# Kernel optimization log

Measured on AMD Instinct MI355X. Metric: run time of the kernel, lower is better.

Reference implementation:

```python
import jax, jax.numpy as jnp
import numpy as np
import math

B, S, D = 1, 1024, 4096
H, HD, KVH = 32, 128, 8
R, FF = 16, 14336
EPS = 1e-5


def setup_inputs() -> dict:
    key = jax.random.key(0)
    ks = jax.random.split(key, 32)
    def nrm(i, shape, scale):
        return jax.random.normal(ks[i], shape, dtype=jnp.float32) * scale
    inp = {}
    inp["x"] = nrm(0, (B, S, D), 0.5)
    inp["norm_w1"] = jnp.ones((D,), jnp.float32)
    inp["norm_w2"] = jnp.ones((D,), jnp.float32)
    # rotary embedding tables (Mistral theta=10000)
    inv_freq = 1.0 / (10000.0 ** (jnp.arange(0, HD, 2, dtype=jnp.float32) / HD))
    freqs = jnp.outer(jnp.arange(S, dtype=jnp.float32), inv_freq)
    emb = jnp.concatenate([freqs, freqs], axis=-1)  # [S, HD]
    inp["cos"] = jnp.cos(emb)
    inp["sin"] = jnp.sin(emb)
    causal = jnp.tril(jnp.ones((S, S), dtype=bool))
    inp["mask"] = jnp.where(causal, 0.0, -1e9).astype(jnp.float32)[None, None]  # [1,1,S,S]
    w_shapes = {"wq": (D, D), "wk": (KVH * HD, D), "wv": (KVH * HD, D),
                "wo": (D, D), "wg": (FF, D), "wu": (FF, D), "wd": (D, FF)}
    i = 1
    for name, shp in w_shapes.items():
        inp[name] = nrm(i, shp, 0.02); i += 1
        dout, din = shp
        inp["la_" + name[1]] = nrm(i, (din, R), 0.02); i += 1
        inp["lb_" + name[1]] = nrm(i, (R, dout), 0.02); i += 1
    inp["num_heads"] = H
    inp["head_dim"] = HD
    inp["num_kv_heads"] = KVH
    return inp


def _rms(x, w):
    # rmsnorm_forward with eps=1e-5, weight only
    return x * jax.lax.rsqrt(jnp.mean(x * x, axis=-1, keepdims=True) + EPS) * w


def _lora(x, W, la, lb):
    # dequantized base weight [out,in] applied as x @ W.T, plus low-rank delta
    return x @ W.T + (x @ la) @ lb


def _rope(x, cos, sin):
    # x: [B, h, S, HD]; rotate_half convention
    x1, x2 = jnp.split(x, 2, axis=-1)
    rot = jnp.concatenate([-x2, x1], axis=-1)
    return x * cos[None, None] + rot * sin[None, None]


def _layer(x, norm_w1, norm_w2, cos, sin, mask,
           wq, la_q, lb_q, wk, la_k, lb_k, wv, la_v, lb_v, wo, la_o, lb_o,
           wg, la_g, lb_g, wu, la_u, lb_u, wd, la_d, lb_d,
           num_heads, head_dim, num_kv_heads):
    b, s, d = x.shape
    n_rep = num_heads // num_kv_heads
    xn1 = _rms(x, norm_w1)
    q = _lora(xn1, wq, la_q, lb_q).reshape(b, s, num_heads, head_dim).transpose(0, 2, 1, 3)
    k = _lora(xn1, wk, la_k, lb_k).reshape(b, s, num_kv_heads, head_dim).transpose(0, 2, 1, 3)
    v = _lora(xn1, wv, la_v, lb_v).reshape(b, s, num_kv_heads, head_dim).transpose(0, 2, 1, 3)
    q = _rope(q, cos, sin)
    k = _rope(k, cos, sin)
    k = jnp.repeat(k, n_rep, axis=1)
    v = jnp.repeat(v, n_rep, axis=1)
    scores = jnp.einsum("bhqd,bhkd->bhqk", q, k) / math.sqrt(head_dim) + mask
    a = jax.nn.softmax(scores, axis=-1)
    o = jnp.einsum("bhqk,bhkd->bhqd", a, v).transpose(0, 2, 1, 3).reshape(b, s, d)
    o = _lora(o, wo, la_o, lb_o)
    x_med = x + o
    xn2 = _rms(x_med, norm_w2)
    gate = _lora(xn2, wg, la_g, lb_g)
    up = _lora(xn2, wu, la_u, lb_u)
    h = jax.nn.silu(gate) * up
    down = _lora(h, wd, la_d, lb_d)
    return x_med + down


def reference(x, norm_w1, norm_w2, cos, sin, mask,
              wq, la_q, lb_q, wk, la_k, lb_k, wv, la_v, lb_v, wo, la_o, lb_o,
              wg, la_g, lb_g, wu, la_u, lb_u, wd, la_d, lb_d,
              num_heads, head_dim, num_kv_heads):
    return _layer(x, norm_w1, norm_w2, cos, sin, mask,
                  wq, la_q, lb_q, wk, la_k, lb_k, wv, la_v, lb_v, wo, la_o, lb_o,
                  wg, la_g, lb_g, wu, la_u, lb_u, wd, la_d, lb_d,
                  num_heads, head_dim, num_kv_heads)
```

## Files before the change

kernel.cpp:

```cpp
#include <hip/hip_runtime.h>
#include <hip/hip_bf16.h>
#include <math.h>

#define SEQ 1024
#define DIM 4096
#define NH 32
#define HD 128
#define NKVH 8
#define FF 14336
#define LR 16

typedef __attribute__((ext_vector_type(8))) short bf16x8;
typedef __attribute__((ext_vector_type(4))) float f32x4;
typedef __attribute__((ext_vector_type(4))) ushort ushort4v;

__device__ __forceinline__ ushort f2bf(float f) {
  union { float f; unsigned u; } v; v.f = f;
  unsigned r = (v.u + 0x7FFFu + ((v.u >> 16) & 1u)) >> 16;
  return (ushort)r;
}
__device__ __forceinline__ float bf2f(ushort h) {
  union { unsigned u; float f; } v; v.u = ((unsigned)h) << 16;
  return v.f;
}

__device__ __forceinline__ void gload_lds16(const void* g, void* l) {
  __builtin_amdgcn_global_load_lds(
      (const __attribute__((address_space(1))) void*)g,
      (__attribute__((address_space(3))) void*)l, 16, 0, 0);
}

__global__ __launch_bounds__(256) void rmsnorm_kernel(const float* __restrict__ x,
                                                      const float* __restrict__ w,
                                                      ushort* __restrict__ out) {
  int row = blockIdx.x;
  int tid = threadIdx.x;
  const float* xr = x + (size_t)row * DIM;
  float vals[16];
  float s = 0.f;
#pragma unroll
  for (int c = 0; c < 4; c++) {
    float4 v = *(const float4*)&xr[(tid + c * 256) * 4];
    vals[c * 4 + 0] = v.x; vals[c * 4 + 1] = v.y;
    vals[c * 4 + 2] = v.z; vals[c * 4 + 3] = v.w;
    s += v.x * v.x + v.y * v.y + v.z * v.z + v.w * v.w;
  }
#pragma unroll
  for (int off = 32; off >= 1; off >>= 1) s += __shfl_down(s, off);
  __shared__ float wsum[4];
  __shared__ float scale_s;
  int lane = tid & 63, wv = tid >> 6;
  if (lane == 0) wsum[wv] = s;
  __syncthreads();
  if (tid == 0) {
    float t = wsum[0] + wsum[1] + wsum[2] + wsum[3];
    scale_s = rsqrtf(t / (float)DIM + 1e-5f);
  }
  __syncthreads();
  float scale = scale_s;
  ushort* orow = out + (size_t)row * DIM;
#pragma unroll
  for (int c = 0; c < 4; c++) {
    int base = (tid + c * 256) * 4;
    float4 wv4 = *(const float4*)&w[base];
    ushort4v ov;
    ov.x = f2bf(vals[c * 4 + 0] * scale * wv4.x);
    ov.y = f2bf(vals[c * 4 + 1] * scale * wv4.y);
    ov.z = f2bf(vals[c * 4 + 2] * scale * wv4.z);
    ov.w = f2bf(vals[c * 4 + 3] * scale * wv4.w);
    *(ushort4v*)&orow[base] = ov;
  }
}

template <int NL>
__global__ __launch_bounds__(256) void lora_a_kernel(
    const ushort* __restrict__ A,
    const float* __restrict__ la0, const float* __restrict__ la1,
    const float* __restrict__ la2,
    ushort* __restrict__ t0, ushort* __restrict__ t1, ushort* __restrict__ t2,
    int K) {
  int m = blockIdx.x, i = threadIdx.x;
  float acc[NL][16];
#pragma unroll
  for (int l = 0; l < NL; l++)
#pragma unroll
    for (int n = 0; n < 16; n++) acc[l][n] = 0.f;

  const ushort* Arow = A + (size_t)m * K;
  int nc = K >> 8;
  for (int c = 0; c < nc; c++) {
    int k = c * 256 + i;
    float a = bf2f(Arow[k]);
#pragma unroll
    for (int l = 0; l < NL; l++) {
      const float* lap = (l == 0 ? la0 : (l == 1 ? la1 : la2)) + (size_t)k * 16;
#pragma unroll
      for (int q = 0; q < 4; q++) {
        float4 lv = *(const float4*)&lap[q * 4];
        acc[l][q * 4 + 0] += a * lv.x;
        acc[l][q * 4 + 1] += a * lv.y;
        acc[l][q * 4 + 2] += a * lv.z;
        acc[l][q * 4 + 3] += a * lv.w;
      }
    }
  }

  __shared__ float red[256][17];
  __shared__ float red2[16][17];
#pragma unroll
  for (int l = 0; l < NL; l++) {
    __syncthreads();
#pragma unroll
    for (int n = 0; n < 16; n++) red[i][n] = acc[l][n];
    __syncthreads();
    {
      int g = i >> 4, n = i & 15;
      float s = 0.f;
#pragma unroll
      for (int j = 0; j < 16; j++) s += red[g * 16 + j][n];
      red2[g][n] = s;
    }
    __syncthreads();
    if (i < 16) {
      float s2 = 0.f;
#pragma unroll
      for (int g2 = 0; g2 < 16; g2++) s2 += red2[g2][i];
      ushort* tp = (l == 0 ? t0 : (l == 1 ? t1 : t2));
      tp[(size_t)m * LR + i] = f2bf(s2);
    }
  }
}

template <int WM>
__global__ __launch_bounds__(512) void gemm256_kernel(
    const ushort* __restrict__ A,
    const float* __restrict__ W0, const float* __restrict__ W1, const float* __restrict__ W2,
    const float* __restrict__ lb0, const float* __restrict__ lb1, const float* __restrict__ lb2,
    const ushort* __restrict__ t0, const ushort* __restrict__ t1, const ushort* __restrict__ t2,
    int c1, int c2, void* __restrict__ outp, int M, int N, int K, int nkp) {
  __shared__ __align__(16) ushort As[2][256 * 64];
  __shared__ __align__(16) ushort Bs[2][256 * 64];
  int tid = threadIdx.x;
  int lane = tid & 63, wave = tid >> 6;
  int wm = wave >> 2, wn = wave & 3;

  int gx = gridDim.x, gy = gridDim.y;
  int flat = blockIdx.x + gx * (blockIdx.y + gy * blockIdx.z);
  int nwg = gx * gy * gridDim.z;
  int q = nwg >> 3, r = nwg & 7;
  int xcd = flat & 7;
  int wgid = (xcd < r ? xcd * (q + 1) : r * (q + 1) + (xcd - r) * q) + (flat >> 3);
  int bx = wgid % gx;
  int tmp = wgid / gx;
  int by = tmp % gy;
  int z = tmp / gy;

  int n0 = bx * 256, m0 = by * 256;
  int k0 = z * nkp;

  const float* Wp; const float* lbp; const ushort* tp; int nseg, wseg;
  if (n0 < c1)      { Wp = W0; lbp = lb0; tp = t0; nseg = n0;      wseg = c1; }
  else if (n0 < c2) { Wp = W1; lbp = lb1; tp = t1; nseg = n0 - c1; wseg = c2 - c1; }
  else              { Wp = W2; lbp = lb2; tp = t2; nseg = n0 - c2; wseg = N - c2; }

  int srow = tid >> 3;
  int sswz = ((tid & 7) ^ (srow & 7)) * 8;
  const ushort* Ab = A + (size_t)(m0 + srow) * K + sswz;
  const float* Wbase = Wp + (size_t)(nseg + srow) * K + (tid & 7) * 8;
  int bphys = ((tid & 7) ^ (srow & 7)) * 8;

  f32x4 acc[8][4] = {};
  float4 breg[8];

#define SHALF(kt, b, h)                                                       \
  _Pragma("unroll") for (int i = 2 * (h); i < 2 * (h) + 2; i++) {             \
    gload_lds16(Ab + (size_t)(i * 64) * K + (size_t)(kt) * 64,                \
                &As[b][wave * 512 + i * 4096]);                               \
  }
#define BLOAD(kt, h)                                                          \
  {                                                                           \
    const float* gp = Wbase + (size_t)((h) * 128) * K + (size_t)(kt) * 64;    \
    breg[(h) * 4 + 0] = *(const float4*)gp;                                   \
    breg[(h) * 4 + 1] = *(const float4*)(gp + 4);                             \
    breg[(h) * 4 + 2] = *(const float4*)(gp + (size_t)64 * K);                \
    breg[(h) * 4 + 3] = *(const float4*)(gp + (size_t)64 * K + 4);            \
  }
#define WRITE_B(b)                                                            \
  _Pragma("unroll") for (int h = 0; h < 2; h++)                               \
  _Pragma("unroll") for (int j = 0; j < 2; j++) {                             \
    int rr = h * 128 + j * 64 + srow;                                         \
    float4 lo = breg[h * 4 + j * 2 + 0];                                      \
    float4 hi = breg[h * 4 + j * 2 + 1];                                      \
    bf16x8 v;                                                                 \
    v[0] = (short)f2bf(lo.x); v[1] = (short)f2bf(lo.y);                       \
    v[2] = (short)f2bf(lo.z); v[3] = (short)f2bf(lo.w);                       \
    v[4] = (short)f2bf(hi.x); v[5] = (short)f2bf(hi.y);                       \
    v[6] = (short)f2bf(hi.z); v[7] = (short)f2bf(hi.w);                       \
    *(bf16x8*)&Bs[b][rr * 64 + (((tid & 7) ^ (rr & 7))) * 8] = v;             \
  }
#define LDFRAG(buf, rr, ks) \
  (*(const bf16x8*)&(buf)[(rr) * 64 + (((ks) * 4 + (lane >> 4)) ^ ((rr) & 7)) * 8])

  BLOAD(k0, 0); BLOAD(k0, 1);
  SHALF(k0, 0, 0); SHALF(k0, 0, 1);
  asm volatile("s_waitcnt vmcnt(4)" ::: "memory");
  WRITE_B(0);
  if (nkp > 1) { BLOAD(k0 + 1, 0); BLOAD(k0 + 1, 1); }
  if (nkp > 1) asm volatile("s_waitcnt vmcnt(8)" ::: "memory");
  else         asm volatile("s_waitcnt vmcnt(0)" ::: "memory");
  asm volatile("s_waitcnt lgkmcnt(0)" ::: "memory");
  __builtin_amdgcn_s_barrier();
  __builtin_amdgcn_sched_barrier(0);

  for (int tau = 0; tau < nkp; tau++) {
    int b = tau & 1;
    bool s1 = (tau + 1 < nkp), s2 = (tau + 2 < nkp);
    const ushort* as = As[b];
    const ushort* bs = Bs[b];
    bf16x8 bfr[4][2];
#pragma unroll
    for (int p = 0; p < 4; p++) {
      bf16x8 af[2][2];
#pragma unroll
      for (int qq = 0; qq < 2; qq++) {
        int ra = wm * 128 + (p * 2 + qq) * 16 + (lane & 15);
#pragma unroll
        for (int ks = 0; ks < 2; ks++) af[qq][ks] = LDFRAG(as, ra, ks);
      }
      if (p == 0) {
#pragma unroll
        for (int f = 0; f < 4; f++) {
          int rb = wn * 64 + f * 16 + (lane & 15);
#pragma unroll
          for (int ks = 0; ks < 2; ks++) bfr[f][ks] = LDFRAG(bs, rb, ks);
        }
      }
      if (p == 0 && s1) { SHALF(k0 + tau + 1, b ^ 1, 0); }
      if (p == 1 && s1) { SHALF(k0 + tau + 1, b ^ 1, 1); }
      if (p == 2 && s2) { BLOAD(k0 + tau + 2, 0); }
      if (p == 3 && s2) { BLOAD(k0 + tau + 2, 1); }
      __builtin_amdgcn_sched_barrier(0);
      __builtin_amdgcn_s_barrier();
      asm volatile("s_waitcnt lgkmcnt(0)" ::: "memory");
      __builtin_amdgcn_sched_barrier(0);
      __builtin_amdgcn_s_setprio(1);
#pragma unroll
      for (int qq = 0; qq < 2; qq++)
#pragma unroll
        for (int fn = 0; fn < 4; fn++)
#pragma unroll
          for (int ks = 0; ks < 2; ks++)
            acc[p * 2 + qq][fn] = __builtin_amdgcn_mfma_f32_16x16x32_bf16(
                af[qq][ks], bfr[fn][ks], acc[p * 2 + qq][fn], 0, 0, 0);
      __builtin_amdgcn_s_setprio(0);
      __builtin_amdgcn_sched_barrier(0);
      if (p == 1 && s1) {
        asm volatile("s_waitcnt vmcnt(4)" ::: "memory");
        WRITE_B(b ^ 1);
        __builtin_amdgcn_sched_barrier(0);
      }
      if (p == 3) {
        if (s2) asm volatile("s_waitcnt vmcnt(8)" ::: "memory");
        else    asm volatile("s_waitcnt vmcnt(0)" ::: "memory");
      }
      __builtin_amdgcn_s_barrier();
      __builtin_amdgcn_sched_barrier(0);
    }
  }
#undef SHALF
#undef BLOAD
#undef WRITE_B

  if (z == 0) {
#pragma unroll
    for (int it = 0; it < 2; it++) {
      int task = tid + it * 512;
      int rr = task >> 2, ls = task & 3;
      int ph = ls ^ (rr & 7);
      bf16x8 avv = {};
      bf16x8 bvv = {};
      if (ls < 2) {
        avv = *(const bf16x8*)&tp[(size_t)(m0 + rr) * LR + ls * 8];
#pragma unroll
        for (int j = 0; j < 8; j++)
          bvv[j] = (short)f2bf(lbp[(size_t)(ls * 8 + j) * wseg + nseg + rr]);
      }
      *(bf16x8*)&As[0][rr * 64 + ph * 8] = avv;
      *(bf16x8*)&Bs[0][rr * 64 + ph * 8] = bvv;
    }
    __syncthreads();
    bf16x8 af[8], bfr[4];
#pragma unroll
    for (int f = 0; f < 8; f++) {
      int ra = wm * 128 + f * 16 + (lane & 15);
      af[f] = LDFRAG(As[0], ra, 0);
    }
#pragma unroll
    for (int f = 0; f < 4; f++) {
      int rb = wn * 64 + f * 16 + (lane & 15);
      bfr[f] = LDFRAG(Bs[0], rb, 0);
    }
#pragma unroll
    for (int fm = 0; fm < 8; fm++)
#pragma unroll
      for (int fn = 0; fn < 4; fn++)
        acc[fm][fn] = __builtin_amdgcn_mfma_f32_16x16x32_bf16(af[fm], bfr[fn], acc[fm][fn], 0, 0, 0);
  }
#undef LDFRAG

#pragma unroll
  for (int fm = 0; fm < 8; fm++) {
#pragma unroll
    for (int j = 0; j < 4; j++) {
      int mg = m0 + wm * 128 + fm * 16 + (lane >> 4) * 4 + j;
#pragma unroll
      for (int fn = 0; fn < 4; fn++) {
        int ng = n0 + wn * 64 + fn * 16 + (lane & 15);
        float v = acc[fm][fn][j];
        if (WM == 0) {
          ((ushort*)outp)[(size_t)mg * N + ng] = f2bf(v);
        } else {
          ((float*)outp)[((size_t)z * M + mg) * (size_t)N + ng] = v;
        }
      }
    }
  }
}

__global__ __launch_bounds__(256) void reduce2_qkv_kernel(const float* __restrict__ p,
                                                          ushort* __restrict__ qb,
                                                          ushort* __restrict__ kb,
                                                          ushort* __restrict__ vtb) {
  size_t i4 = ((size_t)blockIdx.x * 256 + threadIdx.x) * 4;
  size_t sstride = (size_t)SEQ * 6144;
  int m = (int)(i4 / 6144);
  int c = (int)(i4 % 6144);
  float4 a = *(const float4*)&p[i4];
  float4 b = *(const float4*)&p[i4 + sstride];
  float4 s;
  s.x = a.x + b.x; s.y = a.y + b.y; s.z = a.z + b.z; s.w = a.w + b.w;
  if (c < DIM) {
    ushort4v o;
    o.x = f2bf(s.x); o.y = f2bf(s.y); o.z = f2bf(s.z); o.w = f2bf(s.w);
    *(ushort4v*)&qb[(size_t)m * DIM + c] = o;
  } else if (c < DIM + 1024) {
    ushort4v o;
    o.x = f2bf(s.x); o.y = f2bf(s.y); o.z = f2bf(s.z); o.w = f2bf(s.w);
    *(ushort4v*)&kb[(size_t)m * 1024 + (c - DIM)] = o;
  } else {
    int n = c - DIM - 1024;
    vtb[(size_t)(n + 0) * SEQ + m] = f2bf(s.x);
    vtb[(size_t)(n + 1) * SEQ + m] = f2bf(s.y);
    vtb[(size_t)(n + 2) * SEQ + m] = f2bf(s.z);
    vtb[(size_t)(n + 3) * SEQ + m] = f2bf(s.w);
  }
}

__global__ __launch_bounds__(256) void reduce4_res_kernel(const float* __restrict__ p,
                                                          const float* __restrict__ res,
                                                          float* __restrict__ out,
                                                          size_t sstride) {
  size_t i = ((size_t)blockIdx.x * 256 + threadIdx.x) * 4;
  float4 a = *(const float4*)&p[i];
  float4 b = *(const float4*)&p[i + sstride];
  float4 c = *(const float4*)&p[i + 2 * sstride];
  float4 d = *(const float4*)&p[i + 3 * sstride];
  float4 r = *(const float4*)&res[i];
  float4 o;
  o.x = a.x + b.x + c.x + d.x + r.x;
  o.y = a.y + b.y + c.y + d.y + r.y;
  o.z = a.z + b.z + c.z + d.z + r.z;
  o.w = a.w + b.w + c.w + d.w + r.w;
  *(float4*)&out[i] = o;
}

__global__ __launch_bounds__(256) void rope_kernel(ushort* __restrict__ x,
                                                   const float* __restrict__ ct,
                                                   const float* __restrict__ st,
                                                   int nheads, float scale) {
  int idx = blockIdx.x * 256 + threadIdx.x;
  int d = idx & 63;
  int hh = (idx >> 6) % nheads;
  int s = idx / (64 * nheads);
  ushort* p = x + (size_t)s * (nheads * HD) + hh * HD + d;
  float x1 = bf2f(p[0]), x2 = bf2f(p[64]);
  float c = ct[s * HD + d], sn = st[s * HD + d];
  p[0] = f2bf((x1 * c - x2 * sn) * scale);
  p[64] = f2bf((x2 * c + x1 * sn) * scale);
}

__global__ __launch_bounds__(256) void attn_kernel(const ushort* __restrict__ q,
                                                   const ushort* __restrict__ k,
                                                   const ushort* __restrict__ vt,
                                                   ushort* __restrict__ o) {
  int qb = blockIdx.x, h = blockIdx.y, kvh = h >> 2;
  int tid = threadIdx.x, lane = tid & 63, wave = tid >> 6;
  __shared__ ushort Ks[64][136];
  __shared__ ushort Vs[128][72];
  __shared__ ushort Ps[4][16][72];

  bf16x8 qf[4];
  int qrow = qb * 64 + wave * 16 + (lane & 15);
#pragma unroll
  for (int kk = 0; kk < 4; kk++)
    qf[kk] = *(const bf16x8*)&q[(size_t)qrow * DIM + h * HD + kk * 32 + (lane >> 4) * 8];

  f32x4 oacc[8] = {};
  float mrow[4], lrow[4];
  int qr[4];
#pragma unroll
  for (int j = 0; j < 4; j++) {
    mrow[j] = -INFINITY; lrow[j] = 0.f;
    qr[j] = qb * 64 + wave * 16 + (lane >> 4) * 4 + j;
  }

  for (int kt = 0; kt <= qb; kt++) {
    int key0 = kt * 64;
#pragma unroll
    for (int c = 0; c < 4; c++) {
      int e = tid * 32 + c * 8;
      int r = e >> 7, cc = e & 127;
      *(bf16x8*)&Ks[r][cc] =
          *(const bf16x8*)&k[(size_t)(key0 + r) * (NKVH * HD) + kvh * HD + cc];
      int r2 = e >> 6, cc2 = e & 63;
      *(bf16x8*)&Vs[r2][cc2] =
          *(const bf16x8*)&vt[(size_t)(kvh * HD + r2) * SEQ + key0 + cc2];
    }
    __syncthreads();

    f32x4 sf[4] = {};
#pragma unroll
    for (int fn = 0; fn < 4; fn++)
#pragma unroll
      for (int kk = 0; kk < 4; kk++) {
        bf16x8 kf = *(const bf16x8*)&Ks[fn * 16 + (lane & 15)][kk * 32 + (lane >> 4) * 8];
        sf[fn] = __builtin_amdgcn_mfma_f32_16x16x32_bf16(qf[kk], kf, sf[fn], 0, 0, 0);
      }

#pragma unroll
    for (int fn = 0; fn < 4; fn++) {
      int key = key0 + fn * 16 + (lane & 15);
#pragma unroll
      for (int j = 0; j < 4; j++)
        if (key > qr[j]) sf[fn][j] = -INFINITY;
    }

#pragma unroll
    for (int j = 0; j < 4; j++) {
      float mx = fmaxf(fmaxf(sf[0][j], sf[1][j]), fmaxf(sf[2][j], sf[3][j]));
#pragma unroll
      for (int off = 1; off < 16; off <<= 1) mx = fmaxf(mx, __shfl_xor(mx, off));
      float mnew = fmaxf(mrow[j], mx);
      float sc = __expf(mrow[j] - mnew);
      mrow[j] = mnew;
      float rs = 0.f;
#pragma unroll
      for (int fn = 0; fn < 4; fn++) {
        float p = __expf(sf[fn][j] - mnew);
        sf[fn][j] = p;
        rs += p;
      }
#pragma unroll
      for (int off = 1; off < 16; off <<= 1) rs += __shfl_xor(rs, off);
      lrow[j] = lrow[j] * sc + rs;
#pragma unroll
      for (int f2 = 0; f2 < 8; f2++) oacc[f2][j] *= sc;
    }

#pragma unroll
    for (int fn = 0; fn < 4; fn++)
#pragma unroll
      for (int j = 0; j < 4; j++)
        Ps[wave][(lane >> 4) * 4 + j][fn * 16 + (lane & 15)] = f2bf(sf[fn][j]);

#pragma unroll
    for (int kk = 0; kk < 2; kk++) {
      bf16x8 pf = *(const bf16x8*)&Ps[wave][lane & 15][kk * 32 + (lane >> 4) * 8];
#pragma unroll
      for (int f2 = 0; f2 < 8; f2++) {
        bf16x8 vf = *(const bf16x8*)&Vs[f2 * 16 + (lane & 15)][kk * 32 + (lane >> 4) * 8];
        oacc[f2] = __builtin_amdgcn_mfma_f32_16x16x32_bf16(pf, vf, oacc[f2], 0, 0, 0);
      }
    }
    __syncthreads();
  }

#pragma unroll
  for (int j = 0; j < 4; j++) {
    float inv = 1.f / lrow[j];
#pragma unroll
    for (int f2 = 0; f2 < 8; f2++)
      o[(size_t)qr[j] * DIM + h * HD + f2 * 16 + (lane & 15)] = f2bf(oacc[f2][j] * inv);
  }
}

__global__ __launch_bounds__(256) void silu_mul_kernel(const ushort* __restrict__ g,
                                                       const ushort* __restrict__ u,
                                                       ushort* __restrict__ h) {
  size_t idx = (size_t)(blockIdx.x * 256 + threadIdx.x) * 8;
  bf16x8 gv = *(const bf16x8*)&g[idx];
  bf16x8 uv = *(const bf16x8*)&u[idx];
  bf16x8 hv;
#pragma unroll
  for (int i = 0; i < 8; i++) {
    float gf = bf2f((ushort)gv[i]);
    float uf = bf2f((ushort)uv[i]);
    float sv = gf / (1.f + __expf(-gf));
    hv[i] = (short)f2bf(sv * uf);
  }
  *(bf16x8*)&h[idx] = hv;
}

extern "C" void kernel_launch(void* const* d_in, const int* in_sizes, int n_in,
                              void* d_out, int out_size, void* d_ws, size_t ws_size,
                              hipStream_t stream) {
  const float* x    = (const float*)d_in[0];
  const float* w1   = (const float*)d_in[1];
  const float* w2   = (const float*)d_in[2];
  const float* cosT = (const float*)d_in[3];
  const float* sinT = (const float*)d_in[4];
  const float* wq = (const float*)d_in[6];
  const float* la_q = (const float*)d_in[7];
  const float* lb_q = (const float*)d_in[8];
  const float* wk = (const float*)d_in[9];
  const float* la_k = (const float*)d_in[10];
  const float* lb_k = (const float*)d_in[11];
  const float* wv = (const float*)d_in[12];
  const float* la_v = (const float*)d_in[13];
  const float* lb_v = (const float*)d_in[14];
  const float* wo = (const float*)d_in[15];
  const float* la_o = (const float*)d_in[16];
  const float* lb_o = (const float*)d_in[17];
  const float* wg = (const float*)d_in[18];
  const float* la_g = (const float*)d_in[19];
  const float* lb_g = (const float*)d_in[20];
  const float* wu = (const float*)d_in[21];
  const float* la_u = (const float*)d_in[22];
  const float* lb_u = (const float*)d_in[23];
  const float* wd = (const float*)d_in[24];
  const float* la_d = (const float*)d_in[25];
  const float* lb_d = (const float*)d_in[26];
  float* out = (float*)d_out;

  char* ws = (char*)d_ws;
  ushort* xn1 = (ushort*)ws;  ws += (size_t)SEQ * DIM * 2;
  ushort* qb  = (ushort*)ws;  ws += (size_t)SEQ * DIM * 2;
  ushort* kb  = (ushort*)ws;  ws += (size_t)SEQ * NKVH * HD * 2;
  ushort* vtb = (ushort*)ws;  ws += (size_t)SEQ * NKVH * HD * 2;
  ushort* ob  = (ushort*)ws;  ws += (size_t)SEQ * DIM * 2;
  float*  xmed= (float*)ws;   ws += (size_t)SEQ * DIM * 4;
  ushort* xn2 = (ushort*)ws;  ws += (size_t)SEQ * DIM * 2;
  ushort* gate= (ushort*)ws;  ws += (size_t)SEQ * FF * 2;
  ushort* up  = (ushort*)ws;  ws += (size_t)SEQ * FF * 2;
  ushort* hb  = (ushort*)ws;  ws += (size_t)SEQ * FF * 2;
  ushort* t_q = (ushort*)ws; ws += SEQ * LR * 2;
  ushort* t_k = (ushort*)ws; ws += SEQ * LR * 2;
  ushort* t_v = (ushort*)ws; ws += SEQ * LR * 2;
  ushort* t_o = (ushort*)ws; ws += SEQ * LR * 2;
  ushort* t_g = (ushort*)ws; ws += SEQ * LR * 2;
  ushort* t_u = (ushort*)ws; ws += SEQ * LR * 2;
  ushort* t_d = (ushort*)ws; ws += SEQ * LR * 2;

  float* pbuf1 = (float*)gate;
  float* pbuf2 = (float*)xn2;

  size_t snd = (size_t)SEQ * DIM;

  rmsnorm_kernel<<<SEQ, 256, 0, stream>>>(x, w1, xn1);
  lora_a_kernel<3><<<SEQ, 256, 0, stream>>>(xn1, la_q, la_k, la_v, t_q, t_k, t_v, DIM);

  gemm256_kernel<3><<<dim3((DIM + 2048) / 256, SEQ / 256, 2), 512, 0, stream>>>(
      xn1, wq, wk, wv, lb_q, lb_k, lb_v, t_q, t_k, t_v, DIM, DIM + 1024,
      pbuf1, SEQ, DIM + 2048, DIM, 32);
  reduce2_qkv_kernel<<<SEQ * (DIM + 2048) / 1024, 256, 0, stream>>>(pbuf1, qb, kb, vtb);

  rope_kernel<<<SEQ * NH * 64 / 256, 256, 0, stream>>>(qb, cosT, sinT, NH, 0.08838834764831845f);
  rope_kernel<<<SEQ * NKVH * 64 / 256, 256, 0, stream>>>(kb, cosT, sinT, NKVH, 1.0f);
  attn_kernel<<<dim3(SEQ / 64, NH), 256, 0, stream>>>(qb, kb, vtb, ob);

  lora_a_kernel<1><<<SEQ, 256, 0, stream>>>(ob, la_o, la_o, la_o, t_o, t_o, t_o, DIM);
  gemm256_kernel<3><<<dim3(DIM / 256, SEQ / 256, 4), 512, 0, stream>>>(
      ob, wo, wo, wo, lb_o, lb_o, lb_o, t_o, t_o, t_o, DIM, DIM,
      pbuf1, SEQ, DIM, DIM, 16);
  reduce4_res_kernel<<<snd / 1024, 256, 0, stream>>>(pbuf1, x, xmed, snd);

  rmsnorm_kernel<<<SEQ, 256, 0, stream>>>(xmed, w2, xn2);
  lora_a_kernel<2><<<SEQ, 256, 0, stream>>>(xn2, la_g, la_u, la_u, t_g, t_u, t_u, DIM);
  gemm256_kernel<0><<<dim3(FF / 256, SEQ / 256, 1), 512, 0, stream>>>(
      xn2, wg, wg, wg, lb_g, lb_g, lb_g, t_g, t_g, t_g, FF, FF,
      gate, SEQ, FF, DIM, DIM / 64);
  gemm256_kernel<0><<<dim3(FF / 256, SEQ / 256, 1), 512, 0, stream>>>(
      xn2, wu, wu, wu, lb_u, lb_u, lb_u, t_u, t_u, t_u, FF, FF,
      up, SEQ, FF, DIM, DIM / 64);
  silu_mul_kernel<<<SEQ * FF / 8 / 256, 256, 0, stream>>>(gate, up, hb);
  lora_a_kernel<1><<<SEQ, 256, 0, stream>>>(hb, la_d, la_d, la_d, t_d, t_d, t_d, FF);
  gemm256_kernel<3><<<dim3(DIM / 256, SEQ / 256, 4), 512, 0, stream>>>(
      hb, wd, wd, wd, lb_d, lb_d, lb_d, t_d, t_d, t_d, DIM, DIM,
      pbuf2, SEQ, DIM, FF, FF / 4 / 64);
  reduce4_res_kernel<<<snd / 1024, 256, 0, stream>>>(pbuf2, xmed, out, snd);
}
```

Measured before the change: 1.001 ms.

## Fuse RoPE into QKV reduce, RMSNorm into residual reduce, SiLU-mul into up GEMM

The two RoPE kernels are folded into the QKV split-K reduction, and the post-attention residual reduce is merged with the second RMSNorm. The standalone silu_mul kernel is removed: the up-projection GEMM epilogue now reads gate, applies SiLU and writes h directly. The GEMM workgroup-to-tile mapping is also reordered so consecutive workgroups share an N column across M and split-K. Together these cut several kernel launches and full read/write passes over large intermediates, at the cost of a gate read scattered through the GEMM epilogue.

```diff
diff --git a/kernel.cpp b/kernel.cpp
--- a/kernel.cpp
+++ b/kernel.cpp
@@ -137,6 +137,7 @@
     const float* __restrict__ W0, const float* __restrict__ W1, const float* __restrict__ W2,
     const float* __restrict__ lb0, const float* __restrict__ lb1, const float* __restrict__ lb2,
     const ushort* __restrict__ t0, const ushort* __restrict__ t1, const ushort* __restrict__ t2,
+    const ushort* __restrict__ gatep,
     int c1, int c2, void* __restrict__ outp, int M, int N, int K, int nkp) {
   __shared__ __align__(16) ushort As[2][256 * 64];
   __shared__ __align__(16) ushort Bs[2][256 * 64];
@@ -144,16 +145,17 @@
   int lane = tid & 63, wave = tid >> 6;
   int wm = wave >> 2, wn = wave & 3;
 
-  int gx = gridDim.x, gy = gridDim.y;
+  int gx = gridDim.x, gy = gridDim.y, gz = gridDim.z;
   int flat = blockIdx.x + gx * (blockIdx.y + gy * blockIdx.z);
-  int nwg = gx * gy * gridDim.z;
+  int nwg = gx * gy * gz;
   int q = nwg >> 3, r = nwg & 7;
   int xcd = flat & 7;
   int wgid = (xcd < r ? xcd * (q + 1) : r * (q + 1) + (xcd - r) * q) + (flat >> 3);
-  int bx = wgid % gx;
-  int tmp = wgid / gx;
-  int by = tmp % gy;
-  int z = tmp / gy;
+  int sh = gy * gz;
+  int bx = wgid / sh;
+  int rem = wgid - bx * sh;
+  int z = rem / gy;
+  int by = rem - z * gy;
 
   int n0 = bx * 256, m0 = by * 256;
   int k0 = z * nkp;
@@ -167,7 +169,6 @@
   int sswz = ((tid & 7) ^ (srow & 7)) * 8;
   const ushort* Ab = A + (size_t)(m0 + srow) * K + sswz;
   const float* Wbase = Wp + (size_t)(nseg + srow) * K + (tid & 7) * 8;
-  int bphys = ((tid & 7) ^ (srow & 7)) * 8;
 
   f32x4 acc[8][4] = {};
   float4 breg[8];
@@ -319,6 +320,10 @@
         float v = acc[fm][fn][j];
         if (WM == 0) {
           ((ushort*)outp)[(size_t)mg * N + ng] = f2bf(v);
+        } else if (WM == 4) {
+          float g = bf2f(gatep[(size_t)mg * N + ng]);
+          float sv = g / (1.f + __expf(-g));
+          ((ushort*)outp)[(size_t)mg * N + ng] = f2bf(sv * v);
         } else {
           ((float*)outp)[((size_t)z * M + mg) * (size_t)N + ng] = v;
         }
@@ -327,32 +332,57 @@
   }
 }
 
-__global__ __launch_bounds__(256) void reduce2_qkv_kernel(const float* __restrict__ p,
-                                                          ushort* __restrict__ qb,
-                                                          ushort* __restrict__ kb,
-                                                          ushort* __restrict__ vtb) {
-  size_t i4 = ((size_t)blockIdx.x * 256 + threadIdx.x) * 4;
+__global__ __launch_bounds__(256) void reduce2_qkv_rope(const float* __restrict__ p,
+                                                        const float* __restrict__ ct,
+                                                        const float* __restrict__ st,
+                                                        ushort* __restrict__ qb,
+                                                        ushort* __restrict__ kb,
+                                                        ushort* __restrict__ vtb) {
+  int gidx = blockIdx.x * 256 + threadIdx.x;
+  int r = gidx / 896, j = gidx - r * 896;
+  size_t row = (size_t)r * 6144;
   size_t sstride = (size_t)SEQ * 6144;
-  int m = (int)(i4 / 6144);
-  int c = (int)(i4 % 6144);
-  float4 a = *(const float4*)&p[i4];
-  float4 b = *(const float4*)&p[i4 + sstride];
-  float4 s;
-  s.x = a.x + b.x; s.y = a.y + b.y; s.z = a.z + b.z; s.w = a.w + b.w;
-  if (c < DIM) {
-    ushort4v o;
-    o.x = f2bf(s.x); o.y = f2bf(s.y); o.z = f2bf(s.z); o.w = f2bf(s.w);
-    *(ushort4v*)&qb[(size_t)m * DIM + c] = o;
-  } else if (c < DIM + 1024) {
-    ushort4v o;
-    o.x = f2bf(s.x); o.y = f2bf(s.y); o.z = f2bf(s.z); o.w = f2bf(s.w);
-    *(ushort4v*)&kb[(size_t)m * 1024 + (c - DIM)] = o;
+  if (j < 640) {
+    bool isq = j < 512;
+    int jj = isq ? j : j - 512;
+    int h = jj >> 4, d0 = (jj & 15) * 4;
+    size_t base = row + (isq ? 0 : DIM) + h * 128 + d0;
+    float4 a1 = *(const float4*)&p[base];
+    float4 b1 = *(const float4*)&p[base + sstride];
+    float4 a2 = *(const float4*)&p[base + 64];
+    float4 b2 = *(const float4*)&p[base + 64 + sstride];
+    float4 x1, x2;
+    x1.x = a1.x + b1.x; x1.y = a1.y + b1.y; x1.z = a1.z + b1.z; x1.w = a1.w + b1.w;
+    x2.x = a2.x + b2.x; x2.y = a2.y + b2.y; x2.z = a2.z + b2.z; x2.w = a2.w + b2.w;
+    float4 c = *(const float4*)&ct[r * HD + d0];
+    float4 s = *(const float4*)&st[r * HD + d0];
+    float sc = isq ? 0.08838834764831845f : 1.0f;
+    ushort4v o1, o2;
+    o1.x = f2bf((x1.x * c.x - x2.x * s.x) * sc);
+    o1.y = f2bf((x1.y * c.y - x2.y * s.y) * sc);
+    o1.z = f2bf((x1.z * c.z - x2.z * s.z) * sc);
+    o1.w = f2bf((x1.w * c.w - x2.w * s.w) * sc);
+    o2.x = f2bf((x2.x * c.x + x1.x * s.x) * sc);
+    o2.y = f2bf((x2.y * c.y + x1.y * s.y) * sc);
+    o2.z = f2bf((x2.z * c.z + x1.z * s.z) * sc);
+    o2.w = f2bf((x2.w * c.w + x1.w * s.w) * sc);
+    if (isq) {
+      *(ushort4v*)&qb[(size_t)r * DIM + h * 128 + d0] = o1;
+      *(ushort4v*)&qb[(size_t)r * DIM + h * 128 + d0 + 64] = o2;
+    } else {
+      *(ushort4v*)&kb[(size_t)r * 1024 + h * 128 + d0] = o1;
+      *(ushort4v*)&kb[(size_t)r * 1024 + h * 128 + d0 + 64] = o2;
+    }
   } else {
-    int n = c - DIM - 1024;
-    vtb[(size_t)(n + 0) * SEQ + m] = f2bf(s.x);
-    vtb[(size_t)(n + 1) * SEQ + m] = f2bf(s.y);
-    vtb[(size_t)(n + 2) * SEQ + m] = f2bf(s.z);
-    vtb[(size_t)(n + 3) * SEQ + m] = f2bf(s.w);
+    int jj = j - 640;
+    int c0 = jj * 4;
+    size_t base = row + DIM + 1024 + c0;
+    float4 a = *(const float4*)&p[base];
+    float4 b = *(const float4*)&p[base + sstride];
+    vtb[(size_t)(c0 + 0) * SEQ + r] = f2bf(a.x + b.x);
+    vtb[(size_t)(c0 + 1) * SEQ + r] = f2bf(a.y + b.y);
+    vtb[(size_t)(c0 + 2) * SEQ + r] = f2bf(a.z + b.z);
+    vtb[(size_t)(c0 + 3) * SEQ + r] = f2bf(a.w + b.w);
   }
 }
 
@@ -374,19 +404,58 @@
   *(float4*)&out[i] = o;
 }
 
-__global__ __launch_bounds__(256) void rope_kernel(ushort* __restrict__ x,
-                                                   const float* __restrict__ ct,
-                                                   const float* __restrict__ st,
-                                                   int nheads, float scale) {
-  int idx = blockIdx.x * 256 + threadIdx.x;
-  int d = idx & 63;
-  int hh = (idx >> 6) % nheads;
-  int s = idx / (64 * nheads);
-  ushort* p = x + (size_t)s * (nheads * HD) + hh * HD + d;
-  float x1 = bf2f(p[0]), x2 = bf2f(p[64]);
-  float c = ct[s * HD + d], sn = st[s * HD + d];
-  p[0] = f2bf((x1 * c - x2 * sn) * scale);
-  p[64] = f2bf((x2 * c + x1 * sn) * scale);
+__global__ __launch_bounds__(256) void reduce4_res_rms(const float* __restrict__ p,
+                                                       const float* __restrict__ res,
+                                                       const float* __restrict__ w,
+                                                       float* __restrict__ xmed,
+                                                       ushort* __restrict__ xn2,
+                                                       size_t sstride) {
+  int row = blockIdx.x, tid = threadIdx.x;
+  size_t base = (size_t)row * DIM;
+  float vals[16];
+  float sq = 0.f;
+#pragma unroll
+  for (int c = 0; c < 4; c++) {
+    size_t i = base + (tid + c * 256) * 4;
+    float4 a = *(const float4*)&p[i];
+    float4 b = *(const float4*)&p[i + sstride];
+    float4 cc = *(const float4*)&p[i + 2 * sstride];
+    float4 d = *(const float4*)&p[i + 3 * sstride];
+    float4 r = *(const float4*)&res[i];
+    float4 v;
+    v.x = a.x + b.x + cc.x + d.x + r.x;
+    v.y = a.y + b.y + cc.y + d.y + r.y;
+    v.z = a.z + b.z + cc.z + d.z + r.z;
+    v.w = a.w + b.w + cc.w + d.w + r.w;
+    *(float4*)&xmed[i] = v;
+    vals[c * 4 + 0] = v.x; vals[c * 4 + 1] = v.y;
+    vals[c * 4 + 2] = v.z; vals[c * 4 + 3] = v.w;
+    sq += v.x * v.x + v.y * v.y + v.z * v.z + v.w * v.w;
+  }
+#pragma unroll
+  for (int off = 32; off >= 1; off >>= 1) sq += __shfl_down(sq, off);
+  __shared__ float wsum[4];
+  __shared__ float scale_s;
+  int lane = tid & 63, wv = tid >> 6;
+  if (lane == 0) wsum[wv] = sq;
+  __syncthreads();
+  if (tid == 0) {
+    float t = wsum[0] + wsum[1] + wsum[2] + wsum[3];
+    scale_s = rsqrtf(t / (float)DIM + 1e-5f);
+  }
+  __syncthreads();
+  float scale = scale_s;
+#pragma unroll
+  for (int c = 0; c < 4; c++) {
+    int off = (tid + c * 256) * 4;
+    float4 wv4 = *(const float4*)&w[off];
+    ushort4v ov;
+    ov.x = f2bf(vals[c * 4 + 0] * scale * wv4.x);
+    ov.y = f2bf(vals[c * 4 + 1] * scale * wv4.y);
+    ov.z = f2bf(vals[c * 4 + 2] * scale * wv4.z);
+    ov.w = f2bf(vals[c * 4 + 3] * scale * wv4.w);
+    *(ushort4v*)&xn2[base + off] = ov;
+  }
 }
 
 __global__ __launch_bounds__(256) void attn_kernel(const ushort* __restrict__ q,
@@ -492,23 +561,6 @@
     for (int f2 = 0; f2 < 8; f2++)
       o[(size_t)qr[j] * DIM + h * HD + f2 * 16 + (lane & 15)] = f2bf(oacc[f2][j] * inv);
   }
-}
-
-__global__ __launch_bounds__(256) void silu_mul_kernel(const ushort* __restrict__ g,
-                                                       const ushort* __restrict__ u,
-                                                       ushort* __restrict__ h) {
-  size_t idx = (size_t)(blockIdx.x * 256 + threadIdx.x) * 8;
-  bf16x8 gv = *(const bf16x8*)&g[idx];
-  bf16x8 uv = *(const bf16x8*)&u[idx];
-  bf16x8 hv;
-#pragma unroll
-  for (int i = 0; i < 8; i++) {
-    float gf = bf2f((ushort)gv[i]);
-    float uf = bf2f((ushort)uv[i]);
-    float sv = gf / (1.f + __expf(-gf));
-    hv[i] = (short)f2bf(sv * uf);
-  }
-  *(bf16x8*)&h[idx] = hv;
 }
 
 extern "C" void kernel_launch(void* const* d_in, const int* in_sizes, int n_in,
@@ -560,6 +612,7 @@
   ushort* t_g = (ushort*)ws; ws += SEQ * LR * 2;
   ushort* t_u = (ushort*)ws; ws += SEQ * LR * 2;
   ushort* t_d = (ushort*)ws; ws += SEQ * LR * 2;
+  (void)up;
 
   float* pbuf1 = (float*)gate;
   float* pbuf2 = (float*)xn2;
@@ -570,32 +623,28 @@
   lora_a_kernel<3><<<SEQ, 256, 0, stream>>>(xn1, la_q, la_k, la_v, t_q, t_k, t_v, DIM);
 
   gemm256_kernel<3><<<dim3((DIM + 2048) / 256, SEQ / 256, 2), 512, 0, stream>>>(
-      xn1, wq, wk, wv, lb_q, lb_k, lb_v, t_q, t_k, t_v, DIM, DIM + 1024,
+      xn1, wq, wk, wv, lb_q, lb_k, lb_v, t_q, t_k, t_v, nullptr, DIM, DIM + 1024,
       pbuf1, SEQ, DIM + 2048, DIM, 32);
-  reduce2_qkv_kernel<<<SEQ * (DIM + 2048) / 1024, 256, 0, stream>>>(pbuf1, qb, kb, vtb);
-
-  rope_kernel<<<SEQ * NH * 64 / 256, 256, 0, stream>>>(qb, cosT, sinT, NH, 0.08838834764831845f);
-  rope_kernel<<<SEQ * NKVH * 64 / 256, 256, 0, stream>>>(kb, cosT, sinT, NKVH, 1.0f);
+  reduce2_qkv_rope<<<SEQ * 896 / 256, 256, 0, stream>>>(pbuf1, cosT, sinT, qb, kb, vtb);
+
   attn_kernel<<<dim3(SEQ / 64, NH), 256, 0, stream>>>(qb, kb, vtb, ob);
 
   lora_a_kernel<1><<<SEQ, 256, 0, stream>>>(ob, la_o, la_o, la_o, t_o, t_o, t_o, DIM);
   gemm256_kernel<3><<<dim3(DIM / 256, SEQ / 256, 4), 512, 0, stream>>>(
-      ob, wo, wo, wo, lb_o, lb_o, lb_o, t_o, t_o, t_o, DIM, DIM,
+      ob, wo, wo, wo, lb_o, lb_o, lb_o, t_o, t_o, t_o, nullptr, DIM, DIM,
       pbuf1, SEQ, DIM, DIM, 16);
-  reduce4_res_kernel<<<snd / 1024, 256, 0, stream>>>(pbuf1, x, xmed, snd);
-
-  rmsnorm_kernel<<<SEQ, 256, 0, stream>>>(xmed, w2, xn2);
+  reduce4_res_rms<<<SEQ, 256, 0, stream>>>(pbuf1, x, w2, xmed, xn2, snd);
+
   lora_a_kernel<2><<<SEQ, 256, 0, stream>>>(xn2, la_g, la_u, la_u, t_g, t_u, t_u, DIM);
   gemm256_kernel<0><<<dim3(FF / 256, SEQ / 256, 1), 512, 0, stream>>>(
-      xn2, wg, wg, wg, lb_g, lb_g, lb_g, t_g, t_g, t_g, FF, FF,
+      xn2, wg, wg, wg, lb_g, lb_g, lb_g, t_g, t_g, t_g, nullptr, FF, FF,
       gate, SEQ, FF, DIM, DIM / 64);
-  gemm256_kernel<0><<<dim3(FF / 256, SEQ / 256, 1), 512, 0, stream>>>(
-      xn2, wu, wu, wu, lb_u, lb_u, lb_u, t_u, t_u, t_u, FF, FF,
-      up, SEQ, FF, DIM, DIM / 64);
-  silu_mul_kernel<<<SEQ * FF / 8 / 256, 256, 0, stream>>>(gate, up, hb);
+  gemm256_kernel<4><<<dim3(FF / 256, SEQ / 256, 1), 512, 0, stream>>>(
+      xn2, wu, wu, wu, lb_u, lb_u, lb_u, t_u, t_u, t_u, gate, FF, FF,
+      hb, SEQ, FF, DIM, DIM / 64);
   lora_a_kernel<1><<<SEQ, 256, 0, stream>>>(hb, la_d, la_d, la_d, t_d, t_d, t_d, FF);
   gemm256_kernel<3><<<dim3(DIM / 256, SEQ / 256, 4), 512, 0, stream>>>(
-      hb, wd, wd, wd, lb_d, lb_d, lb_d, t_d, t_d, t_d, DIM, DIM,
+      hb, wd, wd, wd, lb_d, lb_d, lb_d, t_d, t_d, t_d, nullptr, DIM, DIM,
       pbuf2, SEQ, DIM, FF, FF / 4 / 64);
   reduce4_res_kernel<<<snd / 1024, 256, 0, stream>>>(pbuf2, xmed, out, snd);
 }
```

Measured after the change: 912.3 us. 8.9% less time.
